# Kernel tuning notes

Measured on AMD Instinct MI355X. Metric: run time of the kernel, lower is better.

Reference implementation:

```python
import jax, jax.numpy as jnp
import numpy as np
from jax import lax

BN_EPS = 1e-5
DN = ('NCHW', 'OIHW', 'NCHW')


def _bn_silu(y, s, b, m, v):
    # eval-mode BatchNorm2d followed by SiLU
    inv = s / jnp.sqrt(v + BN_EPS)
    y = y * inv[None, :, None, None] + (b - m * inv)[None, :, None, None]
    return jax.nn.silu(y)


def _dsconv(x, dw_w, pw_w, s, b, m, v):
    c = x.shape[1]
    y = lax.conv_general_dilated(x, dw_w, (1, 1), [(1, 1), (1, 1)],
                                 dimension_numbers=DN, feature_group_count=c)
    y = lax.conv_general_dilated(y, pw_w, (1, 1), [(0, 0), (0, 0)],
                                 dimension_numbers=DN)
    return _bn_silu(y, s, b, m, v)


def setup_inputs() -> dict:
    key = jax.random.key(0)
    ks = jax.random.split(key, 8)
    B, C, H, W, OUT, TOPK = 32, 256, 64, 64, 256, 2
    CS = C // 2
    inp = {
        'x': jax.random.normal(ks[0], (B, C, H, W), jnp.float32),
        'weights': jax.random.uniform(ks[1], (B, TOPK), jnp.float32),
        'indices': jax.random.randint(ks[2], (B, TOPK), 0, 4),
        'dw_w0': jax.random.normal(ks[3], (CS, 1, 3, 3), jnp.float32) * 0.1,
        'pw_w0': jax.random.normal(ks[4], (OUT, CS, 1, 1), jnp.float32) * 0.05,
        'bn0_s': jnp.ones((OUT,), jnp.float32),
        'bn0_b': jnp.zeros((OUT,), jnp.float32),
        'bn0_m': jnp.zeros((OUT,), jnp.float32),
        'bn0_v': jnp.ones((OUT,), jnp.float32),
        'dw_w1': jax.random.normal(ks[5], (CS, 1, 3, 3), jnp.float32) * 0.1,
        'pw_w1': jax.random.normal(ks[6], (OUT, CS, 1, 1), jnp.float32) * 0.05,
        'bn1_s': jnp.ones((OUT,), jnp.float32),
        'bn1_b': jnp.zeros((OUT,), jnp.float32),
        'bn1_m': jnp.zeros((OUT,), jnp.float32),
        'bn1_v': jnp.ones((OUT,), jnp.float32),
        'w2': jax.random.normal(ks[7], (OUT, C, 1, 1), jnp.float32) * 0.05,
        'bn2_s': jnp.ones((OUT,), jnp.float32),
        'bn2_b': jnp.zeros((OUT,), jnp.float32),
        'bn2_m': jnp.zeros((OUT,), jnp.float32),
        'bn2_v': jnp.ones((OUT,), jnp.float32),
    }
    return inp


def reference(x, weights, indices,
              dw_w0, pw_w0, bn0_s, bn0_b, bn0_m, bn0_v,
              dw_w1, pw_w1, bn1_s, bn1_b, bn1_m, bn1_v,
              w2, bn2_s, bn2_b, bn2_m, bn2_v):
    cs = x.shape[1] // 2
    x_rgb, x_ir = x[:, :cs], x[:, cs:]
    # Per-expert routing coefficient: sum over top-k slots of weight * (index == e).
    # Mathematically identical to the torch masked scatter-add loop.
    def coeff(e):
        return jnp.sum(weights * (indices == e).astype(weights.dtype), axis=1)  # [B]
    e0 = _dsconv(x_rgb, dw_w0, pw_w0, bn0_s, bn0_b, bn0_m, bn0_v)
    e1 = _dsconv(x_ir, dw_w1, pw_w1, bn1_s, bn1_b, bn1_m, bn1_v)
    e2 = _bn_silu(lax.conv_general_dilated(x, w2, (1, 1), [(0, 0), (0, 0)],
                                           dimension_numbers=DN),
                  bn2_s, bn2_b, bn2_m, bn2_v)
    out = (coeff(0)[:, None, None, None] * e0
           + coeff(1)[:, None, None, None] * e1
           + coeff(2)[:, None, None, None] * e2)
    return out
```

## Files before the change

### kernel.cpp

```cpp
#include <hip/hip_runtime.h>

typedef __bf16 bf16x8 __attribute__((ext_vector_type(8)));
typedef float f32x4 __attribute__((ext_vector_type(4)));

#define BN_EPS 1e-5f

__device__ __forceinline__ unsigned short f2bf(float f) {
    union { float f; unsigned u; } x; x.f = f;
    unsigned r = x.u + 0x7fffu + ((x.u >> 16) & 1u);
    return (unsigned short)(r >> 16);
}

__device__ __forceinline__ unsigned pk_bf16(float lo, float hi) {
    unsigned r;
    asm("v_cvt_pk_bf16_f32 %0, %1, %2" : "=v"(r) : "v"(lo), "v"(hi));
    return r;
}

__device__ __forceinline__ float fcomp(float4 v, int j) {
    return (j == 0) ? v.x : (j == 1) ? v.y : (j == 2) ? v.z : v.w;
}

__global__ void prep_kernel(const float* __restrict__ pw0, const float* __restrict__ pw1,
                            const float* __restrict__ w2,
                            const float* __restrict__ s0, const float* __restrict__ b0,
                            const float* __restrict__ m0, const float* __restrict__ v0,
                            const float* __restrict__ s1, const float* __restrict__ b1,
                            const float* __restrict__ m1, const float* __restrict__ v1,
                            const float* __restrict__ s2, const float* __restrict__ b2,
                            const float* __restrict__ m2, const float* __restrict__ v2,
                            unsigned short* __restrict__ wfF0, unsigned short* __restrict__ wfF1,
                            unsigned short* __restrict__ wfF2, float* __restrict__ beta) {
    int o = blockIdx.x;
    int t = threadIdx.x;
    float inv0 = s0[o] * rsqrtf(v0[o] + BN_EPS);
    float inv1 = s1[o] * rsqrtf(v1[o] + BN_EPS);
    float inv2 = s2[o] * rsqrtf(v2[o] + BN_EPS);
    if (t == 0) {
        beta[0 * 256 + o] = b0[o] - m0[o] * inv0;
        beta[1 * 256 + o] = b1[o] - m1[o] * inv1;
        beta[2 * 256 + o] = b2[o] - m2[o] * inv2;
    }
    if (t < 128) {
        wfF0[((t >> 3) * 256 + o) * 8 + (t & 7)] = f2bf(pw0[o * 128 + t] * inv0);
        wfF1[((t >> 3) * 256 + o) * 8 + (t & 7)] = f2bf(pw1[o * 128 + t] * inv1);
    }
    wfF2[((t >> 3) * 256 + o) * 8 + (t & 7)] = f2bf(w2[o * 256 + t] * inv2);
}

template<int NK>
__device__ __forceinline__ void gemm_expert(const char* lds, const unsigned short* __restrict__ W,
                                            int qb, int wave, int l15, int l4,
                                            const int* pxv, const int* swv, f32x4 acc[2][4]) {
    const int row0 = wave * 32 + l15;
    bf16x8 aC[2], bC[4];
#pragma unroll
    for (int ot = 0; ot < 2; ++ot)
        aC[ot] = *(const bf16x8*)(W + (l4 * 256 + row0 + ot * 16) * 8);
#pragma unroll
    for (int tp = 0; tp < 4; ++tp)
        bC[tp] = *(const bf16x8*)(lds + pxv[tp] * 512 + ((qb + l4 * 16) ^ swv[tp]));

#pragma unroll
    for (int kk = 0; kk < NK; ++kk) {
        bf16x8 aN[2], bN[4];
        if (kk + 1 < NK) {
#pragma unroll
            for (int ot = 0; ot < 2; ++ot)
                aN[ot] = *(const bf16x8*)(W + (((kk + 1) * 4 + l4) * 256 + row0 + ot * 16) * 8);
#pragma unroll
            for (int tp = 0; tp < 4; ++tp)
                bN[tp] = *(const bf16x8*)(lds + pxv[tp] * 512 + ((qb + (kk + 1) * 64 + l4 * 16) ^ swv[tp]));
        }
#pragma unroll
        for (int ot = 0; ot < 2; ++ot)
#pragma unroll
            for (int tp = 0; tp < 4; ++tp)
                acc[ot][tp] = __builtin_amdgcn_mfma_f32_16x16x32_bf16(aC[ot], bC[tp], acc[ot][tp], 0, 0, 0);
        if (kk + 1 < NK) {
#pragma unroll
            for (int ot = 0; ot < 2; ++ot) aC[ot] = aN[ot];
#pragma unroll
            for (int tp = 0; tp < 4; ++tp) bC[tp] = bN[tp];
        }
    }
}

__device__ __forceinline__ void epilogue(const f32x4 acc[2][4], float ce, const float* __restrict__ bp,
                                         int wave, int l4, f32x4 res[2][4]) {
#pragma unroll
    for (int ot = 0; ot < 2; ++ot)
#pragma unroll
        for (int j = 0; j < 4; ++j) {
            const int o = wave * 32 + ot * 16 + l4 * 4 + j;
            const float bet = bp[o];
#pragma unroll
            for (int tp = 0; tp < 4; ++tp) {
                float v = acc[ot][tp][j] + bet;
                float sig = __builtin_amdgcn_rcpf(1.f + __expf(-v));
                res[ot][tp][j] += ce * (v * sig);
            }
        }
}

__global__ __launch_bounds__(512, 4)
void fused_kernel(const float* __restrict__ x,
                  const float* __restrict__ wts, const int* __restrict__ idx,
                  const float* __restrict__ dw0, const float* __restrict__ dw1,
                  const unsigned short* __restrict__ wfF0,
                  const unsigned short* __restrict__ wfF1,
                  const unsigned short* __restrict__ wfF2,
                  const float* __restrict__ beta,
                  float* __restrict__ out) {
    __shared__ __align__(16) char lds[69632];

    const int tid  = threadIdx.x;
    const int wave = tid >> 6;
    const int lane = tid & 63;

    const int bid = blockIdx.x;
    const int nb  = ((bid & 7) << 8) | (bid >> 3);
    const int b   = nb >> 6;
    const int h   = nb & 63;

    float c0 = 0.f, c1 = 0.f, c2 = 0.f;
#pragma unroll
    for (int t = 0; t < 2; ++t) {
        int e = idx[b * 2 + t];
        float w = wts[b * 2 + t];
        if (e == 0) c0 += w;
        else if (e == 1) c1 += w;
        else if (e == 2) c2 += w;
    }
    const bool do0 = (c0 != 0.f), do1 = (c1 != 0.f), do2 = (c2 != 0.f);

    const long rowBase = (long)b * 1048576L;

    const int g   = lane >> 2;
    const int kq  = lane & 3;
    const int px0 = g * 4;
    const int l15 = lane & 15;
    const int l4  = lane >> 4;
    const float* xb = x + rowBase + h * 64 + px0;
    const bool hm = (h > 0), hp = (h < 63);

    f32x4 res[2][4];
#pragma unroll
    for (int ot = 0; ot < 2; ++ot)
#pragma unroll
        for (int tp = 0; tp < 4; ++tp)
            res[ot][tp] = (f32x4){0.f, 0.f, 0.f, 0.f};

    int pxv[4], swv[4];
#pragma unroll
    for (int tp = 0; tp < 4; ++tp) {
        pxv[tp] = tp * 16 + l15;
        swv[tp] = (pxv[tp] & 15) << 4;
    }

    const bool dwact = (wave < 4) ? do0 : do1;
    if (dwact || do2) {
#pragma unroll
        for (int i = 0; i < 2; ++i) {
            const int k0 = wave * 32 + i * 16 + kq * 4;
            unsigned dw_p[2][4], rw_p[2][4];
#pragma unroll
            for (int pr = 0; pr < 2; ++pr) {
                float y[2][4];
                float4 rcv[2];
#pragma unroll
                for (int k2 = 0; k2 < 2; ++k2) {
                    const int k = k0 + pr * 2 + k2;
                    const float* xc = xb + (long)k * 4096;
                    float4 rc = *(const float4*)(xc);
                    rcv[k2] = rc;
                    if (dwact) {
                        const float* dwp = (k < 128) ? (dw0 + k * 9) : (dw1 + (k - 128) * 9);
                        float4 rm = hm ? *(const float4*)(xc - 64) : make_float4(0.f, 0.f, 0.f, 0.f);
                        float4 rp = hp ? *(const float4*)(xc + 64) : make_float4(0.f, 0.f, 0.f, 0.f);
                        float lm = __shfl_up(rm.w, 4), lc = __shfl_up(rc.w, 4), lp = __shfl_up(rp.w, 4);
                        float Rm = __shfl_down(rm.x, 4), Rc = __shfl_down(rc.x, 4), Rp = __shfl_down(rp.x, 4);
                        if (g == 0)  { lm = 0.f; lc = 0.f; lp = 0.f; }
                        if (g == 15) { Rm = 0.f; Rc = 0.f; Rp = 0.f; }
                        const float w0 = dwp[0], w1 = dwp[1], w2 = dwp[2];
                        const float w3 = dwp[3], w4 = dwp[4], w5 = dwp[5];
                        const float w6 = dwp[6], w7 = dwp[7], w8 = dwp[8];
                        y[k2][0] = w0*lm   + w1*rm.x + w2*rm.y + w3*lc   + w4*rc.x + w5*rc.y + w6*lp   + w7*rp.x + w8*rp.y;
                        y[k2][1] = w0*rm.x + w1*rm.y + w2*rm.z + w3*rc.x + w4*rc.y + w5*rc.z + w6*rp.x + w7*rp.y + w8*rp.z;
                        y[k2][2] = w0*rm.y + w1*rm.z + w2*rm.w + w3*rc.y + w4*rc.z + w5*rc.w + w6*rp.y + w7*rp.z + w8*rp.w;
                        y[k2][3] = w0*rm.z + w1*rm.w + w2*Rm   + w3*rc.z + w4*rc.w + w5*Rc   + w6*rp.z + w7*rp.w + w8*Rp;
                    }
                }
                if (dwact) {
#pragma unroll
                    for (int j = 0; j < 4; ++j)
                        dw_p[pr][j] = pk_bf16(y[0][j], y[1][j]);
                }
                if (do2) {
#pragma unroll
                    for (int j = 0; j < 4; ++j)
                        rw_p[pr][j] = pk_bf16(fcomp(rcv[0], j), fcomp(rcv[1], j));
                }
            }
            const int colb = (k0 >> 3) * 16;
            const int sub  = (k0 & 4) * 2;
#pragma unroll
            for (int j = 0; j < 4; ++j) {
                const int px  = px0 + j;
                const int off = px * 512 + ((colb ^ ((px & 15) << 4))) + sub;
                if (dwact)
                    *(uint2*)(lds + off) = make_uint2(dw_p[0][j], dw_p[1][j]);
                if (do2)
                    *(uint2*)(lds + 32768 + off) = make_uint2(rw_p[0][j], rw_p[1][j]);
            }
        }
    }
    __syncthreads();

    if (do0) {
        f32x4 acc[2][4];
#pragma unroll
        for (int ot = 0; ot < 2; ++ot)
#pragma unroll
            for (int tp = 0; tp < 4; ++tp) acc[ot][tp] = (f32x4){0.f, 0.f, 0.f, 0.f};
        gemm_expert<4>(lds, wfF0, 0, wave, l15, l4, pxv, swv, acc);
        epilogue(acc, c0, beta, wave, l4, res);
    }
    if (do1) {
        f32x4 acc[2][4];
#pragma unroll
        for (int ot = 0; ot < 2; ++ot)
#pragma unroll
            for (int tp = 0; tp < 4; ++tp) acc[ot][tp] = (f32x4){0.f, 0.f, 0.f, 0.f};
        gemm_expert<4>(lds, wfF1, 256, wave, l15, l4, pxv, swv, acc);
        epilogue(acc, c1, beta + 256, wave, l4, res);
    }
    if (do2) {
        f32x4 acc[2][4];
#pragma unroll
        for (int ot = 0; ot < 2; ++ot)
#pragma unroll
            for (int tp = 0; tp < 4; ++tp) acc[ot][tp] = (f32x4){0.f, 0.f, 0.f, 0.f};
        gemm_expert<8>(lds + 32768, wfF2, 0, wave, l15, l4, pxv, swv, acc);
        epilogue(acc, c2, beta + 512, wave, l4, res);
    }

    float* lf = (float*)lds;
    const long outB = rowBase + h * 64;
    __syncthreads();
    {
        const int reg  = wave >> 2;
        const int rbase = reg * 8704;
#pragma unroll
        for (int ot = 0; ot < 2; ++ot)
#pragma unroll
            for (int j = 0; j < 4; ++j) {
                const int row = (wave & 3) * 32 + ot * 16 + l4 * 4 + j;
#pragma unroll
                for (int tp = 0; tp < 4; ++tp)
                    lf[rbase + row * 68 + tp * 16 + l15] = res[ot][tp][j];
            }
    }
    __syncthreads();
    {
        const int rowq = tid >> 3;
        const int col  = (tid & 7) * 8;
#pragma unroll
        for (int rr = 0; rr < 4; ++rr) {
            const int lr = rowq + rr * 64;
            const int ad = (lr >> 7) * 8704 + (lr & 127) * 68 + col;
            float4 v0 = *(float4*)&lf[ad];
            float4 v1 = *(float4*)&lf[ad + 4];
            float* op = out + outB + (long)lr * 4096 + col;
            *(float4*)op = v0;
            *(float4*)(op + 4) = v1;
        }
    }
}

extern "C" void kernel_launch(void* const* d_in, const int* in_sizes, int n_in,
                              void* d_out, int out_size, void* d_ws, size_t ws_size,
                              hipStream_t stream) {
    const float* x    = (const float*)d_in[0];
    const float* wts  = (const float*)d_in[1];
    const int*   idx  = (const int*)d_in[2];
    const float* dw0  = (const float*)d_in[3];
    const float* pw0  = (const float*)d_in[4];
    const float* s0   = (const float*)d_in[5];
    const float* b0   = (const float*)d_in[6];
    const float* m0   = (const float*)d_in[7];
    const float* v0   = (const float*)d_in[8];
    const float* dw1  = (const float*)d_in[9];
    const float* pw1  = (const float*)d_in[10];
    const float* s1   = (const float*)d_in[11];
    const float* b1   = (const float*)d_in[12];
    const float* m1   = (const float*)d_in[13];
    const float* v1   = (const float*)d_in[14];
    const float* w2   = (const float*)d_in[15];
    const float* s2   = (const float*)d_in[16];
    const float* b2   = (const float*)d_in[17];
    const float* m2   = (const float*)d_in[18];
    const float* v2   = (const float*)d_in[19];

    char* ws = (char*)d_ws;
    unsigned short* wfF0 = (unsigned short*)ws;
    unsigned short* wfF1 = (unsigned short*)(ws + 65536);
    unsigned short* wfF2 = (unsigned short*)(ws + 131072);
    float*          beta = (float*)(ws + 262144);

    prep_kernel<<<256, 256, 0, stream>>>(pw0, pw1, w2,
                                         s0, b0, m0, v0,
                                         s1, b1, m1, v1,
                                         s2, b2, m2, v2,
                                         wfF0, wfF1, wfF2, beta);

    fused_kernel<<<2048, 512, 0, stream>>>(x, wts, idx, dw0, dw1,
                                           wfF0, wfF1, wfF2, beta, (float*)d_out);
}
```

Measured before the change: 93.52 us.

## Prefetch first expert weight fragments early and remap blocks to XCDs by row

The first A-operand weight fragment for each expert GEMM is now loaded before the barrier or before the previous expert's epilogue, so global-load latency overlaps other work. The block-to-(batch,row) mapping also changes so consecutive blocks on one XCD cover different rows of the same batch image, which changes L2 locality of x reads and halo sharing. The cost is extra live registers for the prefetched fragments, and weight loads are issued even for experts that are skipped.

Result: no change. 95.21 us (+1.8%).

```diff
diff --git a/kernel.cpp b/kernel.cpp
--- a/kernel.cpp
+++ b/kernel.cpp
@@ -48,15 +48,21 @@
     wfF2[((t >> 3) * 256 + o) * 8 + (t & 7)] = f2bf(w2[o * 256 + t] * inv2);
 }
 
+__device__ __forceinline__ void loadA0(const unsigned short* __restrict__ W,
+                                       int wave, int l15, int l4, bf16x8 a[2]) {
+    const int row0 = wave * 32 + l15;
+    a[0] = *(const bf16x8*)(W + (l4 * 256 + row0) * 8);
+    a[1] = *(const bf16x8*)(W + (l4 * 256 + row0 + 16) * 8);
+}
+
 template<int NK>
 __device__ __forceinline__ void gemm_expert(const char* lds, const unsigned short* __restrict__ W,
                                             int qb, int wave, int l15, int l4,
-                                            const int* pxv, const int* swv, f32x4 acc[2][4]) {
+                                            const int* pxv, const int* swv,
+                                            const bf16x8 aPre[2], f32x4 acc[2][4]) {
     const int row0 = wave * 32 + l15;
     bf16x8 aC[2], bC[4];
-#pragma unroll
-    for (int ot = 0; ot < 2; ++ot)
-        aC[ot] = *(const bf16x8*)(W + (l4 * 256 + row0 + ot * 16) * 8);
+    aC[0] = aPre[0]; aC[1] = aPre[1];
 #pragma unroll
     for (int tp = 0; tp < 4; ++tp)
         bC[tp] = *(const bf16x8*)(lds + pxv[tp] * 512 + ((qb + l4 * 16) ^ swv[tp]));
@@ -119,9 +125,10 @@
     const int lane = tid & 63;
 
     const int bid = blockIdx.x;
-    const int nb  = ((bid & 7) << 8) | (bid >> 3);
-    const int b   = nb >> 6;
-    const int h   = nb & 63;
+    const int xcd = bid & 7;
+    const int t8  = bid >> 3;
+    const int b   = t8 >> 3;
+    const int h   = ((t8 & 7) << 3) | xcd;
 
     float c0 = 0.f, c1 = 0.f, c2 = 0.f;
 #pragma unroll
@@ -215,33 +222,41 @@
             }
         }
     }
+
+    bf16x8 a0[2];
+    loadA0(wfF0, wave, l15, l4, a0);
+
     __syncthreads();
 
+    f32x4 acc[2][4];
     if (do0) {
-        f32x4 acc[2][4];
 #pragma unroll
         for (int ot = 0; ot < 2; ++ot)
 #pragma unroll
             for (int tp = 0; tp < 4; ++tp) acc[ot][tp] = (f32x4){0.f, 0.f, 0.f, 0.f};
-        gemm_expert<4>(lds, wfF0, 0, wave, l15, l4, pxv, swv, acc);
-        epilogue(acc, c0, beta, wave, l4, res);
-    }
+        gemm_expert<4>(lds, wfF0, 0, wave, l15, l4, pxv, swv, a0, acc);
+    }
+    bf16x8 a1[2];
+    loadA0(wfF1, wave, l15, l4, a1);
+    if (do0) epilogue(acc, c0, beta, wave, l4, res);
+
     if (do1) {
-        f32x4 acc[2][4];
 #pragma unroll
         for (int ot = 0; ot < 2; ++ot)
 #pragma unroll
             for (int tp = 0; tp < 4; ++tp) acc[ot][tp] = (f32x4){0.f, 0.f, 0.f, 0.f};
-        gemm_expert<4>(lds, wfF1, 256, wave, l15, l4, pxv, swv, acc);
-        epilogue(acc, c1, beta + 256, wave, l4, res);
-    }
+        gemm_expert<4>(lds, wfF1, 256, wave, l15, l4, pxv, swv, a1, acc);
+    }
+    bf16x8 a2[2];
+    loadA0(wfF2, wave, l15, l4, a2);
+    if (do1) epilogue(acc, c1, beta + 256, wave, l4, res);
+
     if (do2) {
-        f32x4 acc[2][4];
 #pragma unroll
         for (int ot = 0; ot < 2; ++ot)
 #pragma unroll
             for (int tp = 0; tp < 4; ++tp) acc[ot][tp] = (f32x4){0.f, 0.f, 0.f, 0.f};
-        gemm_expert<8>(lds + 32768, wfF2, 0, wave, l15, l4, pxv, swv, acc);
+        gemm_expert<8>(lds + 32768, wfF2, 0, wave, l15, l4, pxv, swv, a2, acc);
         epilogue(acc, c2, beta + 512, wave, l4, res);
     }
 
```
